# Performance work log

Hardware: AMD Instinct MI355X
Metric: run time of the kernel (lower is better)

The kernel has to match this reference:

```python
import jax, jax.numpy as jnp
import numpy as np

N_USERS = 100000
N_ITEMS = 50000
N_ENT = 80000            # items + tags (tags = 30000)
N_NODES = N_USERS + N_ENT
N_EDGES = 800000
D = 64
N_LAYERS = 2


def _center_net(embs, idx, n, W1, b1, W2, b2):
    # CenterIntersection: linear+relu, linear, segment softmax, weighted segment sum
    act = jnp.maximum(embs @ W1.T + b1, 0.0)
    logits = act @ W2.T + b2
    m = jax.ops.segment_max(logits, idx, num_segments=n)
    e = jnp.exp(logits - m[idx])
    s = jax.ops.segment_sum(e, idx, num_segments=n)
    att = e / s[idx]
    return jax.ops.segment_sum(att * embs, idx, num_segments=n)


def _offset_net(embs, idx, mask, n, use_min, W1, b1, W2, b2):
    # BoxOffsetIntersection restricted to edges where mask is True
    mf = mask[:, None].astype(embs.dtype)
    act = jnp.maximum(embs @ W1.T + b1, 0.0) * mf
    cnt = jax.ops.segment_sum(mask.astype(embs.dtype), idx, num_segments=n)
    mean = jax.ops.segment_sum(act, idx, num_segments=n) / jnp.maximum(cnt, 1.0)[:, None]
    gate = jax.nn.sigmoid(mean @ W2.T + b2)
    if use_min:
        src = jnp.where(mask[:, None], embs, jnp.inf)
        red = jax.ops.segment_min(src, idx, num_segments=n)
    else:
        src = jnp.where(mask[:, None], embs, -jnp.inf)
        red = jax.ops.segment_max(src, idx, num_segments=n)
    red = jnp.where(jnp.isfinite(red), red, 0.0)  # torch_scatter fills empty segments with 0
    return red * gate


def setup_inputs() -> dict:
    key = jax.random.key(0)
    ks = jax.random.split(key, 10)
    s = 0.05  # xavier-like scale
    return {
        "user_emb": jax.random.normal(ks[0], (N_USERS, D), jnp.float32),
        "user_offset_emb": jax.random.normal(ks[1], (N_USERS, D), jnp.float32),
        "item_emb": jax.random.normal(ks[2], (N_ENT, D), jnp.float32),
        "item_offset_emb": jax.random.normal(ks[3], (N_ENT, D), jnp.float32),
        "cW1": jax.random.normal(ks[4], (D, D), jnp.float32) * s,
        "cb1": jnp.zeros((D,), jnp.float32),
        "cW2": jax.random.normal(ks[5], (D, D), jnp.float32) * s,
        "cb2": jnp.zeros((D,), jnp.float32),
        "oW1": jax.random.normal(ks[6], (D, D), jnp.float32) * s,
        "ob1": jnp.zeros((D,), jnp.float32),
        "oW2": jax.random.normal(ks[7], (D, D), jnp.float32) * s,
        "ob2": jnp.zeros((D,), jnp.float32),
        "head": jax.random.randint(ks[8], (N_EDGES,), 0, N_NODES, jnp.int32),
        "tail": jax.random.randint(ks[9], (N_EDGES,), 0, N_NODES, jnp.int32),
    }


def reference(user_emb, user_offset_emb, item_emb, item_offset_emb,
              cW1, cb1, cW2, cb2, oW1, ob1, oW2, ob2, head, tail):
    all_embs = jnp.concatenate([user_emb, item_emb], axis=0)              # [N_NODES, D]
    all_off = jnp.maximum(jnp.concatenate([user_offset_emb, item_offset_emb], axis=0), 0.0)
    uu_idx = jnp.concatenate([jnp.arange(N_USERS), jnp.arange(N_USERS)])
    uu_mask = jnp.ones((2 * N_USERS,), bool)
    m_inter = (tail >= N_USERS) & (head < N_USERS) & (tail < N_USERS + N_ITEMS)
    m_ut = (head < N_USERS) & (tail >= N_USERS + N_ITEMS)
    m_item = (head >= N_USERS) & (head < N_USERS + N_ITEMS)
    m_tag = head >= N_USERS + N_ITEMS
    for _ in range(N_LAYERS):
        h_embs = all_embs[tail]                                           # [E, D] gather
        agg_emb = _center_net(h_embs, head, N_NODES, cW1, cb1, cW2, cb2)
        edge_off = jnp.maximum(all_off[tail], 0.0)                        # [E, D]
        inter_u = _offset_net(edge_off, head, m_inter, N_NODES, True, oW1, ob1, oW2, ob2)[:N_USERS]
        ut_u = _offset_net(edge_off, head, m_ut, N_NODES, False, oW1, ob1, oW2, ob2)[:N_USERS]
        item_o = _offset_net(edge_off, head, m_item, N_NODES, False, oW1, ob1, oW2, ob2)[N_USERS:N_USERS + N_ITEMS]
        tag_o = _offset_net(edge_off, head, m_tag, N_NODES, True, oW1, ob1, oW2, ob2)[N_USERS + N_ITEMS:]
        uo_cat = jnp.concatenate([inter_u, ut_u], axis=0)                 # [2*N_USERS, D]
        user_o = jnp.maximum(_offset_net(uo_cat, uu_idx, uu_mask, N_USERS, False, oW1, ob1, oW2, ob2), 0.0)
        agg_off = jnp.concatenate([user_o, item_o, tag_o], axis=0)
        agg_emb = agg_emb / jnp.maximum(jnp.linalg.norm(agg_emb, axis=1, keepdims=True), 1e-12)  # F.normalize
        all_embs = agg_emb
        all_off = agg_off
    return (all_embs[:N_USERS], all_off[:N_USERS], all_embs[N_USERS:], all_off[N_USERS:])
```

## Files before the change

kernel.cpp:

```cpp
#include <hip/hip_runtime.h>
#include <hip/hip_fp16.h>
#include <math.h>

#define NU 100000
#define NI 50000
#define NENT 80000
#define NN 180000
#define NEDGE 800000
#define SCAN_NB ((NN + 1023) / 1024)
#define UFIN_BLKS ((NU + 63) / 64)
#define EFIN_BLKS (NENT / 64)
#define NODE_BLKS ((NN / 16 + 3) / 4)
#define NU8 (NU * 256)
#define NUI8 ((NU + NI) * 256)

typedef _Float16 f16x4 __attribute__((ext_vector_type(4)));
typedef _Float16 f16x2 __attribute__((ext_vector_type(2)));
typedef float f32x4 __attribute__((ext_vector_type(4)));

__device__ __forceinline__ float sigmoid_f(float x) { return 1.0f / (1.0f + __expf(-x)); }
__device__ __forceinline__ unsigned pack2(float a, float b) {
    __half2 h = __floats2half2_rn(a, b);
    return *(unsigned*)&h;
}
__device__ __forceinline__ f16x2 u2h2(unsigned u) { union { unsigned u; f16x2 h; } x; x.u = u; return x.h; }
__device__ __forceinline__ float fdot2f(f16x2 a, f16x2 b, float c) {
#if __has_builtin(__builtin_amdgcn_fdot2)
    return __builtin_amdgcn_fdot2(a, b, c, false);
#else
    return (float)a[0] * (float)b[0] + (float)a[1] * (float)b[1] + c;
#endif
}
__device__ __forceinline__ _Float16 hminf(_Float16 a, _Float16 b) { return a < b ? a : b; }
__device__ __forceinline__ _Float16 hmaxf(_Float16 a, _Float16 b) { return a > b ? a : b; }

template<typename T>
__device__ __forceinline__ f16x4 ldfrag(const T* __restrict__ p) {
    if constexpr (sizeof(T) == 2) {
        return *(const f16x4*)p;
    } else {
        float4 v = *(const float4*)p;
        f16x4 r; r[0] = (_Float16)v.x; r[1] = (_Float16)v.y; r[2] = (_Float16)v.z; r[3] = (_Float16)v.w;
        return r;
    }
}
template<typename T>
__device__ __forceinline__ f16x4 ldfragr(const T* __restrict__ p) {
    if constexpr (sizeof(T) == 2) {
        f16x4 v = *(const f16x4*)p;
        #pragma unroll
        for (int i = 0; i < 4; ++i) v[i] = hmaxf(v[i], (_Float16)0.f);
        return v;
    } else {
        float4 v = *(const float4*)p;
        f16x4 r;
        r[0] = (_Float16)fmaxf(v.x, 0.f); r[1] = (_Float16)fmaxf(v.y, 0.f);
        r[2] = (_Float16)fmaxf(v.z, 0.f); r[3] = (_Float16)fmaxf(v.w, 0.f);
        return r;
    }
}
__device__ __forceinline__ f16x4 fragp(const _Float16* __restrict__ Wp, int dt, int ks, int lane) {
    return *(const f16x4*)(Wp + (((dt * 4 + ks) * 64 + lane) << 2));
}
__device__ __forceinline__ f32x4 mmw(f16x4 wfrag, f16x4 xfrag, f32x4 c) {
    return __builtin_amdgcn_mfma_f32_16x16x16f16(wfrag, xfrag, c, 0, 0, 0);
}
__device__ __forceinline__ f32x4 bias4(const float* __restrict__ b, int dt, int lk) {
    float4 v = *(const float4*)(b + dt * 16 + lk * 4);
    f32x4 r = {v.x, v.y, v.z, v.w};
    return r;
}

__global__ __launch_bounds__(256) void prep_zero(
    const float* __restrict__ W0, const float* __restrict__ W1,
    const float* __restrict__ W2, const float* __restrict__ W3,
    _Float16* __restrict__ out, int* __restrict__ counts)
{
    int idx = blockIdx.x * 256 + threadIdx.x;
    if (idx < 16384) {
        int mat = idx >> 12, wi = idx & 4095;
        const float* W = (mat == 0) ? W0 : (mat == 1) ? W1 : (mat == 2) ? W2 : W3;
        int tile = wi >> 8;
        int dt = tile >> 2, ks = tile & 3;
        int ln = (wi >> 2) & 63, j = wi & 3;
        int lr = ln & 15, lk = ln >> 4;
        out[idx] = (_Float16)W[(size_t)(dt * 16 + lr) * 64 + ks * 16 + lk * 4 + j];
    }
    int z = idx - 16384;
    if (z >= 0 && z < NN) counts[z] = 0;
}

template<typename T>
__global__ __launch_bounds__(256) void node_pass(
    const T* __restrict__ embU, const T* __restrict__ embE,
    const T* __restrict__ offU, const T* __restrict__ offE,
    const _Float16* __restrict__ cW1f, const float* __restrict__ cb1,
    const _Float16* __restrict__ cW2f, const float* __restrict__ cb2,
    const _Float16* __restrict__ oW1f, const float* __restrict__ ob1,
    unsigned* __restrict__ packedA, unsigned* __restrict__ packedB)
{
    int lane = threadIdx.x & 63, wid = threadIdx.x >> 6;
    int n0 = (blockIdx.x * 4 + wid) * 16;
    if (n0 >= NN) return;
    int lr = lane & 15, lk = lane >> 4;
    const T* eb; const T* ob;
    if (n0 < NU) { eb = embU + (size_t)n0 * 64; ob = offU + (size_t)n0 * 64; }
    else         { eb = embE + (size_t)(n0 - NU) * 64; ob = offE + (size_t)(n0 - NU) * 64; }

    f16x4 ax[4], axo[4];
    #pragma unroll
    for (int ks = 0; ks < 4; ++ks) {
        ax[ks]  = ldfrag(eb + (size_t)lr * 64 + ks * 16 + lk * 4);
        axo[ks] = ldfragr(ob + (size_t)lr * 64 + ks * 16 + lk * 4);
    }
    f32x4 a1c[4];
    #pragma unroll
    for (int dt = 0; dt < 4; ++dt) {
        f32x4 c = bias4(cb1, dt, lk);
        #pragma unroll
        for (int ks = 0; ks < 4; ++ks) c = mmw(fragp(cW1f, dt, ks, lane), ax[ks], c);
        a1c[dt] = c;
    }
    f16x4 a1f[4];
    #pragma unroll
    for (int ks = 0; ks < 4; ++ks)
        #pragma unroll
        for (int r = 0; r < 4; ++r) a1f[ks][r] = (_Float16)fmaxf(a1c[ks][r], 0.f);
    f32x4 lg[4];
    #pragma unroll
    for (int dt = 0; dt < 4; ++dt) {
        f32x4 c = bias4(cb2, dt, lk);
        #pragma unroll
        for (int ks = 0; ks < 4; ++ks) c = mmw(fragp(cW2f, dt, ks, lane), a1f[ks], c);
        lg[dt] = c;
    }
    f32x4 ao[4];
    #pragma unroll
    for (int dt = 0; dt < 4; ++dt) {
        f32x4 c = bias4(ob1, dt, lk);
        #pragma unroll
        for (int ks = 0; ks < 4; ++ks) c = mmw(fragp(oW1f, dt, ks, lane), axo[ks], c);
        ao[dt] = c;
    }
    #pragma unroll
    for (int dt = 0; dt < 4; ++dt) {
        uint4 ua, ub;
        unsigned* pa = &ua.x; unsigned* pb = &ub.x;
        #pragma unroll
        for (int r = 0; r < 4; ++r) {
            float ev = __expf(lg[dt][r]);
            pa[r] = pack2(ev, ev * (float)ax[dt][r]);
            pb[r] = pack2(fmaxf(ao[dt][r], 0.f), (float)axo[dt][r]);
        }
        size_t idx = (size_t)(n0 + lr) * 64 + dt * 16 + lk * 4;
        *(uint4*)(packedA + idx) = ua;
        *(uint4*)(packedB + idx) = ub;
    }
}

__global__ __launch_bounds__(256) void hist_k(const int* __restrict__ head, int* __restrict__ counts) {
    int e = blockIdx.x * 256 + threadIdx.x;
    if (e < NEDGE) atomicAdd(&counts[head[e]], 1);
}

__global__ __launch_bounds__(1024) void scan_local(const int* __restrict__ counts,
                                                   int* __restrict__ excl, int* __restrict__ partials) {
    __shared__ int wsum[16];
    int tid = threadIdx.x, lane = tid & 63, wid = tid >> 6;
    int i = blockIdx.x * 1024 + tid;
    int v = (i < NN) ? counts[i] : 0;
    int s = v;
    #pragma unroll
    for (int d = 1; d < 64; d <<= 1) { int u = __shfl_up(s, d, 64); if (lane >= d) s += u; }
    if (lane == 63) wsum[wid] = s;
    __syncthreads();
    if (wid == 0 && lane < 16) {
        int w = wsum[lane];
        #pragma unroll
        for (int d = 1; d < 16; d <<= 1) { int u = __shfl_up(w, d, 64); if (lane >= d) w += u; }
        wsum[lane] = w;
    }
    __syncthreads();
    int base = wid ? wsum[wid - 1] : 0;
    if (i < NN) excl[i] = base + s - v;
    if (tid == 1023) partials[blockIdx.x] = wsum[15];
}

__global__ __launch_bounds__(256) void scan_carry(const int* __restrict__ partials, int* __restrict__ carries) {
    __shared__ int ws[4];
    int tid = threadIdx.x, lane = tid & 63, wid = tid >> 6;
    int v = (tid < SCAN_NB) ? partials[tid] : 0;
    int s = v;
    #pragma unroll
    for (int d = 1; d < 64; d <<= 1) { int u = __shfl_up(s, d, 64); if (lane >= d) s += u; }
    if (lane == 63) ws[wid] = s;
    __syncthreads();
    int add = 0;
    for (int w = 0; w < wid; ++w) add += ws[w];
    if (tid < SCAN_NB) carries[tid] = add + s - v;
}

__global__ __launch_bounds__(1024) void scan_add(int* __restrict__ excl, const int* __restrict__ carries,
                                                 int* __restrict__ cursor) {
    int i = blockIdx.x * 1024 + threadIdx.x;
    if (i < NN) { int o = excl[i] + carries[blockIdx.x]; excl[i] = o; cursor[i] = o; }
    if (i == 0) excl[NN] = NEDGE;
}

__global__ __launch_bounds__(256) void scatter_k(const int* __restrict__ head, const int* __restrict__ tail,
                                                 int* __restrict__ cursor, int* __restrict__ sorted_t) {
    int e = blockIdx.x * 256 + threadIdx.x;
    if (e < NEDGE) { int pos = atomicAdd(&cursor[head[e]], 1); sorted_t[pos] = tail[e] << 8; }
}

template<bool OUT16>
__global__ __launch_bounds__(256) void seg_pass(
    const unsigned* __restrict__ packedA, const unsigned* __restrict__ packedB,
    const int* __restrict__ offsets, const int* __restrict__ sorted_t,
    void* __restrict__ embOutU_, void* __restrict__ embOutE_,
    _Float16* __restrict__ meanI, _Float16* __restrict__ redI,
    _Float16* __restrict__ meanU, _Float16* __restrict__ redU,
    _Float16* __restrict__ meanE, _Float16* __restrict__ redE)
{
    int lane = threadIdx.x & 63;
    int h = blockIdx.x * 4 + (threadIdx.x >> 6);
    int beg = offsets[h], end = offsets[h + 1];
    bool isUser = (h < NU);
    bool entMin = (h >= NU + NI);
    const f16x2 SEL_LO = {(_Float16)1.0f, (_Float16)0.0f};
    const f16x2 SEL_HI = {(_Float16)0.0f, (_Float16)1.0f};
    float num = 0.f, den = 0.f, s_i = 0.f, s_u = 0.f;
    const _Float16 HINF = u2h2(0x7C007C00u)[0];
    _Float16 m_i = (isUser || entMin) ? HINF : (_Float16)0.f;
    _Float16 m_u = (_Float16)0.f;
    int c_i = 0, c_u = 0;

    const char* pA = (const char*)packedA;
    const char* pB = (const char*)packedB;
    int loff = lane << 2;

#define LOADQ(toff, a, b)                                                       \
    do {                                                                        \
        a = *(const unsigned*)(pA + (size_t)(unsigned)(toff) + loff);           \
        if (!isUser || (toff) >= NU8)                                           \
            b = *(const unsigned*)(pB + (size_t)(unsigned)(toff) + loff);       \
    } while (0)

#define CONSUME(toff, qa, qb)                                                   \
    do {                                                                        \
        f16x2 ea = u2h2(qa);                                                    \
        den = fdot2f(ea, SEL_LO, den);                                          \
        num = fdot2f(ea, SEL_HI, num);                                          \
        if (isUser) {                                                           \
            if ((toff) >= NU8) {                                                \
                f16x2 ab = u2h2(qb);                                            \
                if ((toff) < NUI8) { s_i = fdot2f(ab, SEL_LO, s_i); m_i = hminf(m_i, ab[1]); c_i++; } \
                else               { s_u = fdot2f(ab, SEL_LO, s_u); m_u = hmaxf(m_u, ab[1]); c_u++; } \
            }                                                                   \
        } else {                                                                \
            f16x2 ab = u2h2(qb);                                                \
            s_i = fdot2f(ab, SEL_LO, s_i); c_i++;                               \
            m_i = entMin ? hminf(m_i, ab[1]) : hmaxf(m_i, ab[1]);               \
        }                                                                       \
    } while (0)

    for (int base = beg; base < end; base += 64) {
        int rem = end - base; if (rem > 64) rem = 64;
        int tv = sorted_t[base + (lane < rem ? lane : 0)];
        int tA = 0, tB = 0; unsigned aA = 0, aB = 0, bA = 0, bB = 0;
        tA = __builtin_amdgcn_readlane(tv, 0);
        LOADQ(tA, aA, bA);
        if (rem > 1) { tB = __builtin_amdgcn_readlane(tv, 1); LOADQ(tB, aB, bB); }
        int j = 0;
        for (; j + 2 <= rem; j += 2) {
            CONSUME(tA, aA, bA);
            if (j + 2 < rem) { tA = __builtin_amdgcn_readlane(tv, j + 2); LOADQ(tA, aA, bA); }
            CONSUME(tB, aB, bB);
            if (j + 3 < rem) { tB = __builtin_amdgcn_readlane(tv, j + 3); LOADQ(tB, aB, bB); }
        }
        if (j < rem) CONSUME(tA, aA, bA);
    }
#undef LOADQ
#undef CONSUME

    float v = (den > 0.f) ? num / den : 0.f;
    float sq = v * v;
    #pragma unroll
    for (int m = 32; m; m >>= 1) sq += __shfl_xor(sq, m, 64);
    v = v / fmaxf(sqrtf(sq), 1e-12f);

    float m_if = (float)m_i;
    if (m_if > 1e37f) m_if = 0.f;
    float rc_i = __builtin_amdgcn_rcpf(fmaxf((float)c_i, 1.f));
    if (isUser) {
        size_t r = (size_t)h * 64 + lane;
        if constexpr (OUT16) ((_Float16*)embOutU_)[r] = (_Float16)v;
        else                 ((float*)embOutU_)[r] = v;
        float rc_u = __builtin_amdgcn_rcpf(fmaxf((float)c_u, 1.f));
        meanI[r] = (_Float16)(s_i * rc_i);
        redI[r]  = (_Float16)m_if;
        meanU[r] = (_Float16)(s_u * rc_u);
        redU[r]  = m_u;
    } else {
        size_t r = (size_t)(h - NU) * 64 + lane;
        if constexpr (OUT16) ((_Float16*)embOutE_)[r] = (_Float16)v;
        else                 ((float*)embOutE_)[r] = v;
        meanE[r] = (_Float16)(s_i * rc_i);
        redE[r]  = (_Float16)m_if;
    }
}

template<bool OUT16>
__global__ __launch_bounds__(256) void fin_pass(
    const _Float16* __restrict__ meanI, const _Float16* __restrict__ redI,
    const _Float16* __restrict__ meanU, const _Float16* __restrict__ redU,
    const _Float16* __restrict__ meanE, const _Float16* __restrict__ redE,
    const _Float16* __restrict__ oW1f, const float* __restrict__ ob1,
    const _Float16* __restrict__ oW2f, const float* __restrict__ ob2,
    void* __restrict__ outOffU_, void* __restrict__ entOff_)
{
    int lane = threadIdx.x & 63, wid = threadIdx.x >> 6;
    int lr = lane & 15, lk = lane >> 4;

    if (blockIdx.x >= UFIN_BLKS) {
        int n0 = (((int)blockIdx.x - UFIN_BLKS) * 4 + wid) * 16;
        if (n0 >= NENT) return;
        f16x4 am[4];
        #pragma unroll
        for (int ks = 0; ks < 4; ++ks) am[ks] = *(const f16x4*)(meanE + (size_t)(n0 + lr) * 64 + ks * 16 + lk * 4);
        #pragma unroll
        for (int dt = 0; dt < 4; ++dt) {
            f32x4 c = bias4(ob2, dt, lk);
            #pragma unroll
            for (int ks = 0; ks < 4; ++ks) c = mmw(fragp(oW2f, dt, ks, lane), am[ks], c);
            size_t idx = (size_t)(n0 + lr) * 64 + dt * 16 + lk * 4;
            f16x4 red = *(const f16x4*)(redE + idx);
            if constexpr (OUT16) {
                f16x4 o;
                #pragma unroll
                for (int r = 0; r < 4; ++r) o[r] = (_Float16)((float)red[r] * sigmoid_f(c[r]));
                *(f16x4*)((_Float16*)entOff_ + idx) = o;
            } else {
                float4 o;
                float* po = &o.x;
                #pragma unroll
                for (int r = 0; r < 4; ++r) po[r] = (float)red[r] * sigmoid_f(c[r]);
                *(float4*)((float*)entOff_ + idx) = o;
            }
        }
        return;
    }

    int u0 = (blockIdx.x * 4 + wid) * 16;
    if (u0 >= NU) return;

    f16x4 W1f[4][4], W2f[4][4];
    #pragma unroll
    for (int dt = 0; dt < 4; ++dt)
        #pragma unroll
        for (int ks = 0; ks < 4; ++ks) {
            W1f[dt][ks] = fragp(oW1f, dt, ks, lane);
            W2f[dt][ks] = fragp(oW2f, dt, ks, lane);
        }

    f16x4 am[4];
    f32x4 iu[4], uu[4];
    #pragma unroll
    for (int ks = 0; ks < 4; ++ks) am[ks] = *(const f16x4*)(meanI + (size_t)(u0 + lr) * 64 + ks * 16 + lk * 4);
    #pragma unroll
    for (int dt = 0; dt < 4; ++dt) {
        f32x4 c = bias4(ob2, dt, lk);
        #pragma unroll
        for (int ks = 0; ks < 4; ++ks) c = mmw(W2f[dt][ks], am[ks], c);
        f16x4 red = *(const f16x4*)(redI + (size_t)(u0 + lr) * 64 + dt * 16 + lk * 4);
        #pragma unroll
        for (int r = 0; r < 4; ++r) iu[dt][r] = (float)red[r] * sigmoid_f(c[r]);
    }
    #pragma unroll
    for (int ks = 0; ks < 4; ++ks) am[ks] = *(const f16x4*)(meanU + (size_t)(u0 + lr) * 64 + ks * 16 + lk * 4);
    #pragma unroll
    for (int dt = 0; dt < 4; ++dt) {
        f32x4 c = bias4(ob2, dt, lk);
        #pragma unroll
        for (int ks = 0; ks < 4; ++ks) c = mmw(W2f[dt][ks], am[ks], c);
        f16x4 red = *(const f16x4*)(redU + (size_t)(u0 + lr) * 64 + dt * 16 + lk * 4);
        #pragma unroll
        for (int r = 0; r < 4; ++r) uu[dt][r] = (float)red[r] * sigmoid_f(c[r]);
    }
    f16x4 iuf[4], uuf[4];
    #pragma unroll
    for (int ks = 0; ks < 4; ++ks)
        #pragma unroll
        for (int r = 0; r < 4; ++r) { iuf[ks][r] = (_Float16)iu[ks][r]; uuf[ks][r] = (_Float16)uu[ks][r]; }
    f32x4 mn[4];
    #pragma unroll
    for (int dt = 0; dt < 4; ++dt) {
        f32x4 c = bias4(ob1, dt, lk);
        #pragma unroll
        for (int ks = 0; ks < 4; ++ks) c = mmw(W1f[dt][ks], iuf[ks], c);
        #pragma unroll
        for (int r = 0; r < 4; ++r) mn[dt][r] = fmaxf(c[r], 0.f);
    }
    #pragma unroll
    for (int dt = 0; dt < 4; ++dt) {
        f32x4 c = bias4(ob1, dt, lk);
        #pragma unroll
        for (int ks = 0; ks < 4; ++ks) c = mmw(W1f[dt][ks], uuf[ks], c);
        #pragma unroll
        for (int r = 0; r < 4; ++r) mn[dt][r] = 0.5f * (mn[dt][r] + fmaxf(c[r], 0.f));
    }
    f16x4 mnf[4];
    #pragma unroll
    for (int ks = 0; ks < 4; ++ks)
        #pragma unroll
        for (int r = 0; r < 4; ++r) mnf[ks][r] = (_Float16)mn[ks][r];
    #pragma unroll
    for (int dt = 0; dt < 4; ++dt) {
        f32x4 c = bias4(ob2, dt, lk);
        #pragma unroll
        for (int ks = 0; ks < 4; ++ks) c = mmw(W2f[dt][ks], mnf[ks], c);
        size_t idx = (size_t)(u0 + lr) * 64 + dt * 16 + lk * 4;
        if constexpr (OUT16) {
            f16x4 o;
            #pragma unroll
            for (int r = 0; r < 4; ++r)
                o[r] = (_Float16)fmaxf(fmaxf(iu[dt][r], uu[dt][r]) * sigmoid_f(c[r]), 0.f);
            *(f16x4*)((_Float16*)outOffU_ + idx) = o;
        } else {
            float4 o;
            float* po = &o.x;
            #pragma unroll
            for (int r = 0; r < 4; ++r)
                po[r] = fmaxf(fmaxf(iu[dt][r], uu[dt][r]) * sigmoid_f(c[r]), 0.f);
            *(float4*)((float*)outOffU_ + idx) = o;
        }
    }
}

extern "C" void kernel_launch(void* const* d_in, const int* in_sizes, int n_in,
                              void* d_out, int out_size, void* d_ws, size_t ws_size,
                              hipStream_t stream)
{
    const float* user_emb = (const float*)d_in[0];
    const float* user_off = (const float*)d_in[1];
    const float* item_emb = (const float*)d_in[2];
    const float* item_off = (const float*)d_in[3];
    const float* cW1 = (const float*)d_in[4];
    const float* cb1 = (const float*)d_in[5];
    const float* cW2 = (const float*)d_in[6];
    const float* cb2 = (const float*)d_in[7];
    const float* oW1 = (const float*)d_in[8];
    const float* ob1 = (const float*)d_in[9];
    const float* oW2 = (const float*)d_in[10];
    const float* ob2 = (const float*)d_in[11];
    const int* head = (const int*)d_in[12];
    const int* tail = (const int*)d_in[13];
    float* out = (float*)d_out;

    const size_t SZ = (size_t)NN * 64;
    _Float16* A16   = (_Float16*)d_ws;
    _Float16* B16   = A16 + SZ;
    unsigned* packedA = (unsigned*)(B16 + SZ);
    unsigned* packedB = packedA + SZ;
    _Float16* meanI_h = (_Float16*)(packedB + SZ);
    _Float16* redI_h  = meanI_h + (size_t)NU * 64;
    _Float16* meanU_h = redI_h + (size_t)NU * 64;
    _Float16* redU_h  = meanU_h + (size_t)NU * 64;
    _Float16* meanE_h = redU_h + (size_t)NU * 64;
    _Float16* redE_h  = meanE_h + (size_t)NENT * 64;
    _Float16* wpre    = redE_h + (size_t)NENT * 64;
    int* counts   = (int*)(wpre + 4 * 4096);
    int* offsets  = counts + NN;
    int* cursor   = offsets + NN + 1;
    int* sorted_t = cursor + NN;
    int* partials = sorted_t + NEDGE;
    int* carries  = partials + SCAN_NB;

    const _Float16* cW1f = wpre;
    const _Float16* cW2f = wpre + 4096;
    const _Float16* oW1f = wpre + 8192;
    const _Float16* oW2f = wpre + 12288;

    prep_zero<<<64 + (NN + 255) / 256, 256, 0, stream>>>(cW1, cW2, oW1, oW2,
                                                         (_Float16*)wpre, counts);
    hist_k<<<(NEDGE + 255) / 256, 256, 0, stream>>>(head, counts);
    scan_local<<<SCAN_NB, 1024, 0, stream>>>(counts, offsets, partials);
    scan_carry<<<1, 256, 0, stream>>>(partials, carries);
    scan_add<<<SCAN_NB, 1024, 0, stream>>>(offsets, carries, cursor);
    scatter_k<<<(NEDGE + 255) / 256, 256, 0, stream>>>(head, tail, cursor, sorted_t);

    node_pass<float><<<NODE_BLKS, 256, 0, stream>>>(
        user_emb, item_emb, user_off, item_off,
        cW1f, cb1, cW2f, cb2, oW1f, ob1, packedA, packedB);
    seg_pass<true><<<NN / 4, 256, 0, stream>>>(
        packedA, packedB, offsets, sorted_t,
        A16, A16 + (size_t)NU * 64,
        meanI_h, redI_h, meanU_h, redU_h, meanE_h, redE_h);
    fin_pass<true><<<UFIN_BLKS + EFIN_BLKS, 256, 0, stream>>>(
        meanI_h, redI_h, meanU_h, redU_h, meanE_h, redE_h,
        oW1f, ob1, oW2f, ob2, B16, B16 + (size_t)NU * 64);

    node_pass<_Float16><<<NODE_BLKS, 256, 0, stream>>>(
        A16, A16 + (size_t)NU * 64, B16, B16 + (size_t)NU * 64,
        cW1f, cb1, cW2f, cb2, oW1f, ob1, packedA, packedB);
    seg_pass<false><<<NN / 4, 256, 0, stream>>>(
        packedA, packedB, offsets, sorted_t,
        out, out + (size_t)2 * NU * 64,
        meanI_h, redI_h, meanU_h, redU_h, meanE_h, redE_h);
    fin_pass<false><<<UFIN_BLKS + EFIN_BLKS, 256, 0, stream>>>(
        meanI_h, redI_h, meanU_h, redU_h, meanE_h, redE_h,
        oW1f, ob1, oW2f, ob2, out + (size_t)NU * 64, out + ((size_t)2 * NU + NENT) * 64);
}
```

Measured before the change: 415.3 us.

## Bucket user edges by tail class to remove per-edge branching in segment pass

The CSR build now sorts edges into sub-buckets: each user node gets three buckets (user, item and tag tails) and each entity node gets one. The segment pass then runs one specialised loop per bucket through a templated helper, so there are no per-edge class checks and no per-edge counters, and edges with user tails skip the offset load entirely. In exchange, the bucket array is larger (380k instead of 180k entries), the scan needs a 1024-thread carry kernel, and the histogram and scatter kernels also have to read the tail array.

After: 424.7 us. 1.02x slower.

```diff
diff --git a/kernel.cpp b/kernel.cpp
--- a/kernel.cpp
+++ b/kernel.cpp
@@ -7,12 +7,11 @@
 #define NENT 80000
 #define NN 180000
 #define NEDGE 800000
-#define SCAN_NB ((NN + 1023) / 1024)
+#define NB (3 * NU + NENT)
+#define SCAN_NB ((NB + 1023) / 1024)
 #define UFIN_BLKS ((NU + 63) / 64)
 #define EFIN_BLKS (NENT / 64)
 #define NODE_BLKS ((NN / 16 + 3) / 4)
-#define NU8 (NU * 256)
-#define NUI8 ((NU + NI) * 256)
 
 typedef _Float16 f16x4 __attribute__((ext_vector_type(4)));
 typedef _Float16 f16x2 __attribute__((ext_vector_type(2)));
@@ -69,6 +68,10 @@
     float4 v = *(const float4*)(b + dt * 16 + lk * 4);
     f32x4 r = {v.x, v.y, v.z, v.w};
     return r;
+}
+__device__ __forceinline__ int bucket_of(int h, int t) {
+    if (h < NU) return h * 3 + ((t < NU) ? 0 : (t < NU + NI) ? 1 : 2);
+    return 3 * NU + (h - NU);
 }
 
 __global__ __launch_bounds__(256) void prep_zero(
@@ -87,7 +90,7 @@
         out[idx] = (_Float16)W[(size_t)(dt * 16 + lr) * 64 + ks * 16 + lk * 4 + j];
     }
     int z = idx - 16384;
-    if (z >= 0 && z < NN) counts[z] = 0;
+    if (z >= 0 && z < NB) counts[z] = 0;
 }
 
 template<typename T>
@@ -158,9 +161,10 @@
     }
 }
 
-__global__ __launch_bounds__(256) void hist_k(const int* __restrict__ head, int* __restrict__ counts) {
+__global__ __launch_bounds__(256) void hist_k(const int* __restrict__ head, const int* __restrict__ tail,
+                                              int* __restrict__ counts) {
     int e = blockIdx.x * 256 + threadIdx.x;
-    if (e < NEDGE) atomicAdd(&counts[head[e]], 1);
+    if (e < NEDGE) atomicAdd(&counts[bucket_of(head[e], tail[e])], 1);
 }
 
 __global__ __launch_bounds__(1024) void scan_local(const int* __restrict__ counts,
@@ -168,7 +172,7 @@
     __shared__ int wsum[16];
     int tid = threadIdx.x, lane = tid & 63, wid = tid >> 6;
     int i = blockIdx.x * 1024 + tid;
-    int v = (i < NN) ? counts[i] : 0;
+    int v = (i < NB) ? counts[i] : 0;
     int s = v;
     #pragma unroll
     for (int d = 1; d < 64; d <<= 1) { int u = __shfl_up(s, d, 64); if (lane >= d) s += u; }
@@ -182,35 +186,88 @@
     }
     __syncthreads();
     int base = wid ? wsum[wid - 1] : 0;
-    if (i < NN) excl[i] = base + s - v;
+    if (i < NB) excl[i] = base + s - v;
     if (tid == 1023) partials[blockIdx.x] = wsum[15];
 }
 
-__global__ __launch_bounds__(256) void scan_carry(const int* __restrict__ partials, int* __restrict__ carries) {
-    __shared__ int ws[4];
+__global__ __launch_bounds__(1024) void scan_carry(const int* __restrict__ partials, int* __restrict__ carries) {
+    __shared__ int wsum[16];
     int tid = threadIdx.x, lane = tid & 63, wid = tid >> 6;
     int v = (tid < SCAN_NB) ? partials[tid] : 0;
     int s = v;
     #pragma unroll
     for (int d = 1; d < 64; d <<= 1) { int u = __shfl_up(s, d, 64); if (lane >= d) s += u; }
-    if (lane == 63) ws[wid] = s;
+    if (lane == 63) wsum[wid] = s;
     __syncthreads();
-    int add = 0;
-    for (int w = 0; w < wid; ++w) add += ws[w];
-    if (tid < SCAN_NB) carries[tid] = add + s - v;
+    if (wid == 0 && lane < 16) {
+        int w = wsum[lane];
+        #pragma unroll
+        for (int d = 1; d < 16; d <<= 1) { int u = __shfl_up(w, d, 64); if (lane >= d) w += u; }
+        wsum[lane] = w;
+    }
+    __syncthreads();
+    int base = wid ? wsum[wid - 1] : 0;
+    if (tid < SCAN_NB) carries[tid] = base + s - v;
 }
 
 __global__ __launch_bounds__(1024) void scan_add(int* __restrict__ excl, const int* __restrict__ carries,
                                                  int* __restrict__ cursor) {
     int i = blockIdx.x * 1024 + threadIdx.x;
-    if (i < NN) { int o = excl[i] + carries[blockIdx.x]; excl[i] = o; cursor[i] = o; }
-    if (i == 0) excl[NN] = NEDGE;
+    if (i < NB) { int o = excl[i] + carries[blockIdx.x]; excl[i] = o; cursor[i] = o; }
+    if (i == 0) excl[NB] = NEDGE;
 }
 
 __global__ __launch_bounds__(256) void scatter_k(const int* __restrict__ head, const int* __restrict__ tail,
                                                  int* __restrict__ cursor, int* __restrict__ sorted_t) {
     int e = blockIdx.x * 256 + threadIdx.x;
-    if (e < NEDGE) { int pos = atomicAdd(&cursor[head[e]], 1); sorted_t[pos] = tail[e] << 8; }
+    if (e < NEDGE) {
+        int pos = atomicAdd(&cursor[bucket_of(head[e], tail[e])], 1);
+        sorted_t[pos] = tail[e] << 8;
+    }
+}
+
+template<int CLS>
+__device__ __forceinline__ void run_seg(
+    const char* __restrict__ pA, const char* __restrict__ pB,
+    const int* __restrict__ sorted_t, int beg, int end, int loff, int lane,
+    float& den, float& num, float& s, _Float16& m)
+{
+    const f16x2 SEL_LO = {(_Float16)1.0f, (_Float16)0.0f};
+    const f16x2 SEL_HI = {(_Float16)0.0f, (_Float16)1.0f};
+#define LOADQ(toff, a, b)                                                       \
+    do {                                                                        \
+        a = *(const unsigned*)(pA + (size_t)(unsigned)(toff) + loff);           \
+        if (CLS) b = *(const unsigned*)(pB + (size_t)(unsigned)(toff) + loff);  \
+    } while (0)
+#define CONSUME(qa, qb)                                                         \
+    do {                                                                        \
+        f16x2 ea = u2h2(qa);                                                    \
+        den = fdot2f(ea, SEL_LO, den);                                          \
+        num = fdot2f(ea, SEL_HI, num);                                          \
+        if (CLS) {                                                              \
+            f16x2 ab = u2h2(qb);                                                \
+            s = fdot2f(ab, SEL_LO, s);                                          \
+            m = (CLS == 1) ? hminf(m, ab[1]) : hmaxf(m, ab[1]);                 \
+        }                                                                       \
+    } while (0)
+    for (int base = beg; base < end; base += 64) {
+        int rem = end - base; if (rem > 64) rem = 64;
+        int tv = sorted_t[base + (lane < rem ? lane : 0)];
+        int tA, tB; unsigned aA = 0, aB = 0, bA = 0, bB = 0;
+        tA = __builtin_amdgcn_readlane(tv, 0);
+        LOADQ(tA, aA, bA);
+        if (rem > 1) { tB = __builtin_amdgcn_readlane(tv, 1); LOADQ(tB, aB, bB); }
+        int j = 0;
+        for (; j + 2 <= rem; j += 2) {
+            CONSUME(aA, bA);
+            if (j + 2 < rem) { tA = __builtin_amdgcn_readlane(tv, j + 2); LOADQ(tA, aA, bA); }
+            CONSUME(aB, bB);
+            if (j + 3 < rem) { tB = __builtin_amdgcn_readlane(tv, j + 3); LOADQ(tB, aB, bB); }
+        }
+        if (j < rem) CONSUME(aA, bA);
+    }
+#undef LOADQ
+#undef CONSUME
 }
 
 template<bool OUT16>
@@ -224,64 +281,32 @@
 {
     int lane = threadIdx.x & 63;
     int h = blockIdx.x * 4 + (threadIdx.x >> 6);
-    int beg = offsets[h], end = offsets[h + 1];
     bool isUser = (h < NU);
     bool entMin = (h >= NU + NI);
-    const f16x2 SEL_LO = {(_Float16)1.0f, (_Float16)0.0f};
-    const f16x2 SEL_HI = {(_Float16)0.0f, (_Float16)1.0f};
     float num = 0.f, den = 0.f, s_i = 0.f, s_u = 0.f;
     const _Float16 HINF = u2h2(0x7C007C00u)[0];
     _Float16 m_i = (isUser || entMin) ? HINF : (_Float16)0.f;
     _Float16 m_u = (_Float16)0.f;
-    int c_i = 0, c_u = 0;
+    float c_i, c_u = 0.f;
 
     const char* pA = (const char*)packedA;
     const char* pB = (const char*)packedB;
     int loff = lane << 2;
 
-#define LOADQ(toff, a, b)                                                       \
-    do {                                                                        \
-        a = *(const unsigned*)(pA + (size_t)(unsigned)(toff) + loff);           \
-        if (!isUser || (toff) >= NU8)                                           \
-            b = *(const unsigned*)(pB + (size_t)(unsigned)(toff) + loff);       \
-    } while (0)
-
-#define CONSUME(toff, qa, qb)                                                   \
-    do {                                                                        \
-        f16x2 ea = u2h2(qa);                                                    \
-        den = fdot2f(ea, SEL_LO, den);                                          \
-        num = fdot2f(ea, SEL_HI, num);                                          \
-        if (isUser) {                                                           \
-            if ((toff) >= NU8) {                                                \
-                f16x2 ab = u2h2(qb);                                            \
-                if ((toff) < NUI8) { s_i = fdot2f(ab, SEL_LO, s_i); m_i = hminf(m_i, ab[1]); c_i++; } \
-                else               { s_u = fdot2f(ab, SEL_LO, s_u); m_u = hmaxf(m_u, ab[1]); c_u++; } \
-            }                                                                   \
-        } else {                                                                \
-            f16x2 ab = u2h2(qb);                                                \
-            s_i = fdot2f(ab, SEL_LO, s_i); c_i++;                               \
-            m_i = entMin ? hminf(m_i, ab[1]) : hmaxf(m_i, ab[1]);               \
-        }                                                                       \
-    } while (0)
-
-    for (int base = beg; base < end; base += 64) {
-        int rem = end - base; if (rem > 64) rem = 64;
-        int tv = sorted_t[base + (lane < rem ? lane : 0)];
-        int tA = 0, tB = 0; unsigned aA = 0, aB = 0, bA = 0, bB = 0;
-        tA = __builtin_amdgcn_readlane(tv, 0);
-        LOADQ(tA, aA, bA);
-        if (rem > 1) { tB = __builtin_amdgcn_readlane(tv, 1); LOADQ(tB, aB, bB); }
-        int j = 0;
-        for (; j + 2 <= rem; j += 2) {
-            CONSUME(tA, aA, bA);
-            if (j + 2 < rem) { tA = __builtin_amdgcn_readlane(tv, j + 2); LOADQ(tA, aA, bA); }
-            CONSUME(tB, aB, bB);
-            if (j + 3 < rem) { tB = __builtin_amdgcn_readlane(tv, j + 3); LOADQ(tB, aB, bB); }
-        }
-        if (j < rem) CONSUME(tA, aA, bA);
-    }
-#undef LOADQ
-#undef CONSUME
+    if (isUser) {
+        int o0 = offsets[3 * h], o1 = offsets[3 * h + 1];
+        int o2 = offsets[3 * h + 2], o3 = offsets[3 * h + 3];
+        run_seg<0>(pA, pB, sorted_t, o0, o1, loff, lane, den, num, s_i, m_i);
+        run_seg<1>(pA, pB, sorted_t, o1, o2, loff, lane, den, num, s_i, m_i);
+        run_seg<2>(pA, pB, sorted_t, o2, o3, loff, lane, den, num, s_u, m_u);
+        c_i = (float)(o2 - o1); c_u = (float)(o3 - o2);
+    } else {
+        int b = 3 * NU + (h - NU);
+        int o0 = offsets[b], o1 = offsets[b + 1];
+        if (entMin) run_seg<1>(pA, pB, sorted_t, o0, o1, loff, lane, den, num, s_i, m_i);
+        else        run_seg<2>(pA, pB, sorted_t, o0, o1, loff, lane, den, num, s_i, m_i);
+        c_i = (float)(o1 - o0);
+    }
 
     float v = (den > 0.f) ? num / den : 0.f;
     float sq = v * v;
@@ -291,12 +316,12 @@
 
     float m_if = (float)m_i;
     if (m_if > 1e37f) m_if = 0.f;
-    float rc_i = __builtin_amdgcn_rcpf(fmaxf((float)c_i, 1.f));
+    float rc_i = __builtin_amdgcn_rcpf(fmaxf(c_i, 1.f));
     if (isUser) {
         size_t r = (size_t)h * 64 + lane;
         if constexpr (OUT16) ((_Float16*)embOutU_)[r] = (_Float16)v;
         else                 ((float*)embOutU_)[r] = v;
-        float rc_u = __builtin_amdgcn_rcpf(fmaxf((float)c_u, 1.f));
+        float rc_u = __builtin_amdgcn_rcpf(fmaxf(c_u, 1.f));
         meanI[r] = (_Float16)(s_i * rc_i);
         redI[r]  = (_Float16)m_if;
         meanU[r] = (_Float16)(s_u * rc_u);
@@ -470,9 +495,9 @@
     _Float16* redE_h  = meanE_h + (size_t)NENT * 64;
     _Float16* wpre    = redE_h + (size_t)NENT * 64;
     int* counts   = (int*)(wpre + 4 * 4096);
-    int* offsets  = counts + NN;
-    int* cursor   = offsets + NN + 1;
-    int* sorted_t = cursor + NN;
+    int* offsets  = counts + NB;
+    int* cursor   = offsets + NB + 1;
+    int* sorted_t = cursor + NB;
     int* partials = sorted_t + NEDGE;
     int* carries  = partials + SCAN_NB;
 
@@ -481,11 +506,11 @@
     const _Float16* oW1f = wpre + 8192;
     const _Float16* oW2f = wpre + 12288;
 
-    prep_zero<<<64 + (NN + 255) / 256, 256, 0, stream>>>(cW1, cW2, oW1, oW2,
+    prep_zero<<<64 + (NB + 255) / 256, 256, 0, stream>>>(cW1, cW2, oW1, oW2,
                                                          (_Float16*)wpre, counts);
-    hist_k<<<(NEDGE + 255) / 256, 256, 0, stream>>>(head, counts);
+    hist_k<<<(NEDGE + 255) / 256, 256, 0, stream>>>(head, tail, counts);
     scan_local<<<SCAN_NB, 1024, 0, stream>>>(counts, offsets, partials);
-    scan_carry<<<1, 256, 0, stream>>>(partials, carries);
+    scan_carry<<<1, 1024, 0, stream>>>(partials, carries);
     scan_add<<<SCAN_NB, 1024, 0, stream>>>(offsets, carries, cursor);
     scatter_k<<<(NEDGE + 255) / 256, 256, 0, stream>>>(head, tail, cursor, sorted_t);
 
```
